# Kernel optimization log

Hardware: AMD Instinct MI355X
Metric: run time of the kernel (lower is better)

## Reference

```python
import jax, jax.numpy as jnp
import numpy as np

N_NODES = 50000
N_RAND_EDGES = 575000  # plus N_NODES self loops -> 625000 total edges
C = 128


def setup_inputs() -> dict:
    key = jax.random.key(0)
    ks = jax.random.split(key, 7)
    x = jax.random.normal(ks[0], (N_NODES, C), dtype=jnp.float32)
    er = jax.random.randint(ks[1], (2, N_RAND_EDGES), 0, N_NODES)
    loops = jnp.arange(N_NODES)
    edge_index = jnp.concatenate([er, jnp.stack([loops, loops])], axis=1)  # [2, E]
    E = edge_index.shape[1]
    edge_feature = jax.random.randint(ks[2], (E, 3), 0, 2)  # in-range for all 3 tables
    glorot = lambda k, shp: jax.random.uniform(k, shp, jnp.float32, -1.0, 1.0) * jnp.sqrt(6.0 / (shp[0] + shp[1]))
    weight = glorot(ks[3], (C, C))
    emb0 = glorot(ks[4], (5, C))
    emb1 = glorot(ks[5], (6, C))
    emb2 = glorot(ks[6], (2, C))
    return {"x": x, "edge_index": edge_index, "edge_feature": edge_feature,
            "weight": weight, "emb0": emb0, "emb1": emb1, "emb2": emb2}


def reference(x, edge_index, edge_feature, weight, emb0, emb1, emb2):
    n = x.shape[0]
    xw = x @ weight  # [N, C]
    # BondEncoder: sum of per-column embeddings -> [E, C]
    ef = emb0[edge_feature[:, 0]] + emb1[edge_feature[:, 1]] + emb2[edge_feature[:, 2]]
    row, col = edge_index[0], edge_index[1]
    # GCN symmetric normalization (graph already contains all self loops)
    deg = jax.ops.segment_sum(jnp.ones(row.shape[0], xw.dtype), row, num_segments=n)
    dinv = jnp.where(deg > 0, jax.lax.rsqrt(deg), 0.0)
    norm = dinv[row] * dinv[col]  # [E]
    # message: norm * (x_j + edge_feature); aggregate: scatter-add at target
    msg = norm[:, None] * (xw[row] + ef)  # [E, C]
    out = jax.ops.segment_sum(msg, col, num_segments=n)  # [N, C]
    return out
```

## Files before the change

kernel.cpp:

```cpp
#include <hip/hip_runtime.h>

#define CC 128
#define NB_HIST 96
#define MAXNW 12512
typedef unsigned short ushort_t;
typedef unsigned int uint_t;
typedef __attribute__((ext_vector_type(8))) short short8_t;
typedef __attribute__((ext_vector_type(4))) float float4_t;

__device__ __forceinline__ ushort_t f2bf(float f) {
    uint_t u = __float_as_uint(f);
    u = (u + 0x7FFFu + ((u >> 16) & 1u)) >> 16;
    return (ushort_t)u;
}
#define BF_LO(u) __uint_as_float((u) << 16)
#define BF_HI(u) __uint_as_float((u) & 0xFFFF0000u)

__global__ void prep_kernel(const float* __restrict__ w, ushort_t* __restrict__ wbt,
                            const float* __restrict__ emb0, const float* __restrict__ emb1,
                            const float* __restrict__ emb2, ushort_t* __restrict__ cmb) {
    if (blockIdx.x < 64) {
        const int i = blockIdx.x * 256 + threadIdx.x;
        const int nn = i >> 7, k = i & 127;
        wbt[i] = f2bf(w[k * CC + nn]);
    } else {
        const int c = blockIdx.x - 64;
        const int t = threadIdx.x;
        if (c < 60 && t < CC) {
            const int i0 = c / 12, j0 = (c % 12) / 2, k0 = c % 2;
            cmb[c * CC + t] = f2bf(emb0[i0 * CC + t] + emb1[j0 * CC + t] + emb2[k0 * CC + t]);
        }
    }
}

__global__ __launch_bounds__(256) void xw_kernel(const float* __restrict__ x,
                                                 const ushort_t* __restrict__ wbt,
                                                 ushort_t* __restrict__ xwb, int n) {
    const int wave = threadIdx.x >> 6;
    const int lane = threadIdx.x & 63;
    const int row0 = blockIdx.x * 64 + wave * 16;
    const int r  = lane & 15;
    const int kb = lane >> 4;
    const int arow = row0 + r;
    const bool rok = arow < n;

    float4_t acc[8];
    #pragma unroll
    for (int t = 0; t < 8; ++t) acc[t] = (float4_t){0.f, 0.f, 0.f, 0.f};

    #pragma unroll
    for (int ks = 0; ks < 4; ++ks) {
        short8_t ahi, alo;
        if (rok) {
            const float* xp = &x[(size_t)arow * CC + ks * 32 + kb * 8];
            const float4 x0 = *reinterpret_cast<const float4*>(xp);
            const float4 x1 = *reinterpret_cast<const float4*>(xp + 4);
            const float xv[8] = {x0.x, x0.y, x0.z, x0.w, x1.x, x1.y, x1.z, x1.w};
            #pragma unroll
            for (int i = 0; i < 8; ++i) {
                const ushort_t h = f2bf(xv[i]);
                ahi[i] = (short)h;
                const float hf = __uint_as_float((uint_t)h << 16);
                alo[i] = (short)f2bf(xv[i] - hf);
            }
        } else {
            #pragma unroll
            for (int i = 0; i < 8; ++i) { ahi[i] = 0; alo[i] = 0; }
        }
        #pragma unroll
        for (int nt = 0; nt < 8; ++nt) {
            const short8_t b = *reinterpret_cast<const short8_t*>(
                &wbt[(size_t)(nt * 16 + r) * CC + ks * 32 + kb * 8]);
            acc[nt] = __builtin_amdgcn_mfma_f32_16x16x32_bf16(alo, b, acc[nt], 0, 0, 0);
            acc[nt] = __builtin_amdgcn_mfma_f32_16x16x32_bf16(ahi, b, acc[nt], 0, 0, 0);
        }
    }
    #pragma unroll
    for (int reg = 0; reg < 4; ++reg) {
        const int orow = row0 + kb * 4 + reg;
        if (orow < n) {
            #pragma unroll
            for (int nt = 0; nt < 8; ++nt)
                xwb[(size_t)orow * CC + nt * 16 + r] = f2bf(acc[nt][reg]);
        }
    }
}

__global__ __launch_bounds__(1024) void hist2_kernel(const int* __restrict__ ei,
                                                     uint_t* __restrict__ bufr,
                                                     uint_t* __restrict__ bufc,
                                                     int E, int nw) {
    __shared__ uint_t hr[MAXNW];
    __shared__ uint_t hc[MAXNW];
    const int tid = threadIdx.x;
    for (int i = tid; i < nw; i += 1024) { hr[i] = 0u; hc[i] = 0u; }
    __syncthreads();
    const int chunk = (E + NB_HIST - 1) / NB_HIST;
    const int beg = blockIdx.x * chunk;
    const int end = min(E, beg + chunk);
    for (int i = beg + tid; i < end; i += 2048) {
        const int i1 = i + 1024;
        const bool ok1 = i1 < end;
        const int r0 = ei[i], c0 = ei[E + i];
        int r1 = 0, c1 = 0;
        if (ok1) { r1 = ei[i1]; c1 = ei[E + i1]; }
        atomicAdd(&hr[r0 >> 2], 1u << ((r0 & 3) * 8));
        atomicAdd(&hc[c0 >> 2], 1u << ((c0 & 3) * 8));
        if (ok1) {
            atomicAdd(&hr[r1 >> 2], 1u << ((r1 & 3) * 8));
            atomicAdd(&hc[c1 >> 2], 1u << ((c1 & 3) * 8));
        }
    }
    __syncthreads();
    uint_t* obr = &bufr[(size_t)blockIdx.x * nw];
    uint_t* obc = &bufc[(size_t)blockIdx.x * nw];
    for (int i = tid; i < nw; i += 1024) { obr[i] = hr[i]; obc[i] = hc[i]; }
}

__global__ void hscan_kernel(uint_t* __restrict__ bufr, uint_t* __restrict__ bufc,
                             float* __restrict__ dinv, int* __restrict__ cnt_col,
                             int* __restrict__ bsum, int nbw, int nw, int n) {
    const int t = threadIdx.x;
    if ((int)blockIdx.x < nbw) {
        const int w = blockIdx.x * 256 + t;
        if (w >= nw) return;
        uint_t s = 0;
        #pragma unroll 4
        for (int b = 0; b < NB_HIST; ++b) s += bufr[(size_t)b * nw + w];
        const int base = w * 4;
        float4 o;
        o.x = (s & 0xFFu)         ? rsqrtf((float)(s & 0xFFu)) : 0.f;
        o.y = ((s >> 8) & 0xFFu)  ? rsqrtf((float)((s >> 8) & 0xFFu)) : 0.f;
        o.z = ((s >> 16) & 0xFFu) ? rsqrtf((float)((s >> 16) & 0xFFu)) : 0.f;
        o.w = (s >> 24)           ? rsqrtf((float)(s >> 24)) : 0.f;
        if (base + 3 < n) *reinterpret_cast<float4*>(&dinv[base]) = o;
        else {
            if (base < n) dinv[base] = o.x;
            if (base + 1 < n) dinv[base + 1] = o.y;
            if (base + 2 < n) dinv[base + 2] = o.z;
        }
    } else {
        const int w = (blockIdx.x - nbw) * 256 + t;
        int tot = 0;
        if (w < nw) {
            uint_t s = 0;
            for (int b = 0; b < NB_HIST; ++b) {
                const size_t idx = (size_t)b * nw + w;
                const uint_t u = bufc[idx];
                bufc[idx] = s;
                s += u;
            }
            const int base = w * 4;
            int4 o;
            o.x = (int)(s & 0xFFu);
            o.y = (int)((s >> 8) & 0xFFu);
            o.z = (int)((s >> 16) & 0xFFu);
            o.w = (int)(s >> 24);
            if (base + 3 < n) { *reinterpret_cast<int4*>(&cnt_col[base]) = o; tot = o.x + o.y + o.z + o.w; }
            else {
                if (base < n) { cnt_col[base] = o.x; tot += o.x; }
                if (base + 1 < n) { cnt_col[base + 1] = o.y; tot += o.y; }
                if (base + 2 < n) { cnt_col[base + 2] = o.z; tot += o.z; }
            }
        }
        #pragma unroll
        for (int d = 32; d; d >>= 1) tot += __shfl_down(tot, d);
        __shared__ int wsum[4];
        if ((t & 63) == 0) wsum[t >> 6] = tot;
        __syncthreads();
        if (t == 0) bsum[blockIdx.x - nbw] = wsum[0] + wsum[1] + wsum[2] + wsum[3];
    }
}

__global__ void bscan_kernel(const int* __restrict__ bsum, int* __restrict__ boff,
                             int nb, int* __restrict__ offs, int n) {
    __shared__ int tmp[256];
    const int t = threadIdx.x;
    int v = (t < nb) ? bsum[t] : 0;
    tmp[t] = v; __syncthreads();
    for (int d = 1; d < 256; d <<= 1) {
        int u = (t >= d) ? tmp[t - d] : 0; __syncthreads();
        tmp[t] += u; __syncthreads();
    }
    if (t < nb) boff[t] = tmp[t] - v;
    if (t == 255) offs[n] = tmp[255];
}

__global__ void offs_kernel(const int* __restrict__ cnt, const int* __restrict__ boff,
                            int* __restrict__ offs, int* __restrict__ next, int nw, int n) {
    __shared__ int tmp[256];
    const int t = threadIdx.x;
    const int w = blockIdx.x * 256 + t;
    int4 c4 = {0, 0, 0, 0};
    const int base = w * 4;
    if (w < nw) {
        if (base + 3 < n) c4 = *reinterpret_cast<const int4*>(&cnt[base]);
        else {
            if (base < n) c4.x = cnt[base];
            if (base + 1 < n) c4.y = cnt[base + 1];
            if (base + 2 < n) c4.z = cnt[base + 2];
        }
    }
    const int tot = c4.x + c4.y + c4.z + c4.w;
    tmp[t] = tot; __syncthreads();
    for (int d = 1; d < 256; d <<= 1) {
        int u = (t >= d) ? tmp[t - d] : 0; __syncthreads();
        tmp[t] += u; __syncthreads();
    }
    if (w < nw) {
        int e = boff[blockIdx.x] + tmp[t] - tot;
        int4 o;
        o.x = e; o.y = e + c4.x; o.z = o.y + c4.y; o.w = o.z + c4.z;
        if (base + 3 < n) {
            *reinterpret_cast<int4*>(&offs[base]) = o;
            *reinterpret_cast<int4*>(&next[base]) = o;
        } else {
            if (base < n) { offs[base] = o.x; next[base] = o.x; }
            if (base + 1 < n) { offs[base + 1] = o.y; next[base + 1] = o.y; }
            if (base + 2 < n) { offs[base + 2] = o.z; next[base + 2] = o.z; }
        }
    }
}

__global__ __launch_bounds__(1024) void fill_kernel(const int* __restrict__ ei,
                                                    const int* __restrict__ ef,
                                                    const float* __restrict__ dinv,
                                                    const uint_t* __restrict__ bufc,
                                                    const int* __restrict__ offs,
                                                    int2* __restrict__ sc, int E, int nw) {
    __shared__ uint_t cur[MAXNW];
    const int tid = threadIdx.x;
    for (int i = tid; i < nw; i += 1024) cur[i] = 0u;
    __syncthreads();
    const int chunk = (E + NB_HIST - 1) / NB_HIST;
    const int beg = blockIdx.x * chunk;
    const int end = min(E, beg + chunk);
    const uint_t* myb = &bufc[(size_t)blockIdx.x * nw];
    for (int i0 = beg + tid; i0 < end; i0 += 4096) {
        int  ii[4]; bool ok[4];
        int  r4[4], c4[4], code4[4], pos4[4];
        float dv4[4];
        #pragma unroll
        for (int u = 0; u < 4; ++u) { ii[u] = i0 + u * 1024; ok[u] = ii[u] < end; }
        #pragma unroll
        for (int u = 0; u < 4; ++u) if (ok[u]) { r4[u] = ei[ii[u]]; c4[u] = ei[E + ii[u]]; }
        #pragma unroll
        for (int u = 0; u < 4; ++u) if (ok[u])
            code4[u] = ef[ii[u] * 3 + 0] * 12 + ef[ii[u] * 3 + 1] * 2 + ef[ii[u] * 3 + 2];
        #pragma unroll
        for (int u = 0; u < 4; ++u) if (ok[u]) dv4[u] = dinv[r4[u]];
        #pragma unroll
        for (int u = 0; u < 4; ++u) if (ok[u]) {
            const int c = c4[u];
            const int sh = (c & 3) * 8;
            const uint_t old = atomicAdd(&cur[c >> 2], 1u << sh);
            const int rank = (int)((old >> sh) & 0xFFu);
            const int cum = (int)((myb[c >> 2] >> sh) & 0xFFu);
            pos4[u] = offs[c] + cum + rank;
        }
        #pragma unroll
        for (int u = 0; u < 4; ++u) if (ok[u])
            sc[pos4[u]] = make_int2(r4[u] | (code4[u] << 16), __float_as_int(dv4[u]));
    }
}

__global__ void fill_glob_kernel(const int* __restrict__ ei, const int* __restrict__ ef,
                                 const float* __restrict__ dinv, int* __restrict__ next,
                                 int2* __restrict__ sc, int E) {
    int i = blockIdx.x * blockDim.x + threadIdx.x;
    int stride = gridDim.x * blockDim.x;
    for (; i < E; i += stride) {
        int r = ei[i];
        int c = ei[E + i];
        int pos = atomicAdd(&next[c], 1);
        int code = ef[i * 3 + 0] * 12 + ef[i * 3 + 1] * 2 + ef[i * 3 + 2];
        sc[pos] = make_int2(r | (code << 16), __float_as_int(dinv[r]));
    }
}

__global__ void hist_kernel(const int* __restrict__ ei, int* __restrict__ cnt_row,
                            int* __restrict__ cnt_col, int E) {
    int i = blockIdx.x * blockDim.x + threadIdx.x;
    int stride = gridDim.x * blockDim.x;
    for (; i < E; i += stride) {
        atomicAdd(&cnt_row[ei[i]], 1);
        atomicAdd(&cnt_col[ei[E + i]], 1);
    }
}
__global__ void dinv_kernel(const int* __restrict__ cnt_row, float* __restrict__ dinv, int n) {
    int i = blockIdx.x * blockDim.x + threadIdx.x;
    if (i < n) {
        int d = cnt_row[i];
        dinv[i] = (d > 0) ? rsqrtf((float)d) : 0.0f;
    }
}
__global__ void blocksum2_kernel(const int* __restrict__ cnt, int* __restrict__ bsum,
                                 int nw, int n) {
    const int t = threadIdx.x;
    const int w = blockIdx.x * 256 + t;
    int tot = 0;
    const int base = w * 4;
    if (w < nw) {
        for (int k = 0; k < 4; ++k) if (base + k < n) tot += cnt[base + k];
    }
    #pragma unroll
    for (int d = 32; d; d >>= 1) tot += __shfl_down(tot, d);
    __shared__ int wsum[4];
    if ((t & 63) == 0) wsum[t >> 6] = tot;
    __syncthreads();
    if (t == 0) bsum[blockIdx.x] = wsum[0] + wsum[1] + wsum[2] + wsum[3];
}

__global__ void gather_kernel(const ushort_t* __restrict__ xwb, const int2* __restrict__ sc,
                              const int* __restrict__ offs, const float* __restrict__ dinv,
                              const ushort_t* __restrict__ cmb, float* __restrict__ out, int n) {
    const int v = blockIdx.x * 4 + (threadIdx.x >> 6);
    if (v >= n) return;
    const int lane = threadIdx.x & 63;
    const int g = lane >> 4;
    const int l16 = lane & 15;
    const int end = offs[v + 1];

    float a[8];
    #pragma unroll
    for (int k = 0; k < 8; ++k) a[k] = 0.f;

    int jj = offs[v] + g;
    int2 e = (jj < end) ? sc[jj] : make_int2(0, 0);
    while (jj < end) {
        const int2 en = (jj + 4 < end) ? sc[jj + 4] : make_int2(0, 0);
        const int r_ = e.x & 0xFFFF, c_ = e.x >> 16;
        const float w_ = __int_as_float(e.y);
        const uint4 ux = *reinterpret_cast<const uint4*>(&xwb[(size_t)r_ * CC + l16 * 8]);
        const uint4 uc = *reinterpret_cast<const uint4*>(&cmb[c_ * CC + l16 * 8]);
        a[0] += w_ * (BF_LO(ux.x) + BF_LO(uc.x));
        a[1] += w_ * (BF_HI(ux.x) + BF_HI(uc.x));
        a[2] += w_ * (BF_LO(ux.y) + BF_LO(uc.y));
        a[3] += w_ * (BF_HI(ux.y) + BF_HI(uc.y));
        a[4] += w_ * (BF_LO(ux.z) + BF_LO(uc.z));
        a[5] += w_ * (BF_HI(ux.z) + BF_HI(uc.z));
        a[6] += w_ * (BF_LO(ux.w) + BF_LO(uc.w));
        a[7] += w_ * (BF_HI(ux.w) + BF_HI(uc.w));
        e = en;
        jj += 4;
    }
    #pragma unroll
    for (int k = 0; k < 8; ++k) {
        a[k] += __shfl_xor(a[k], 16);
        a[k] += __shfl_xor(a[k], 32);
    }
    if (g == 0) {
        const float s = dinv[v];
        float4 o0 = make_float4(s * a[0], s * a[1], s * a[2], s * a[3]);
        float4 o1 = make_float4(s * a[4], s * a[5], s * a[6], s * a[7]);
        float* op = &out[(size_t)v * CC + l16 * 8];
        *reinterpret_cast<float4*>(op) = o0;
        *reinterpret_cast<float4*>(op + 4) = o1;
    }
}

extern "C" void kernel_launch(void* const* d_in, const int* in_sizes, int n_in,
                              void* d_out, int out_size, void* d_ws, size_t ws_size,
                              hipStream_t stream) {
    const float* x      = (const float*)d_in[0];
    const int*   ei     = (const int*)d_in[1];
    const int*   ef     = (const int*)d_in[2];
    const float* weight = (const float*)d_in[3];
    const float* emb0   = (const float*)d_in[4];
    const float* emb1   = (const float*)d_in[5];
    const float* emb2   = (const float*)d_in[6];
    float* out = (float*)d_out;

    const int n = in_sizes[0] / CC;
    const int E = in_sizes[1] / 2;
    const int nw = (n + 3) / 4;
    const int nbw = (nw + 255) / 256;

    char* p = (char*)d_ws;
    auto alloc = [&](size_t bytes) {
        char* r = p;
        p += (bytes + 63) & ~(size_t)63;
        return r;
    };
    ushort_t* xwb   = (ushort_t*)alloc((size_t)n * CC * sizeof(ushort_t));
    ushort_t* wbt   = (ushort_t*)alloc(CC * CC * sizeof(ushort_t));
    ushort_t* cmb   = (ushort_t*)alloc(60 * CC * sizeof(ushort_t));
    float* dinv     = (float*)alloc(n * sizeof(float));
    int*   cnt_row  = (int*)alloc((size_t)n * sizeof(int));
    int*   cnt_col  = (int*)alloc((size_t)n * sizeof(int));
    int*   offs     = (int*)alloc((n + 1) * sizeof(int));
    int*   next     = (int*)alloc((size_t)n * sizeof(int));
    int*   bsum     = (int*)alloc(nbw * sizeof(int));
    int*   boff     = (int*)alloc(nbw * sizeof(int));
    int2*  sc       = (int2*)alloc((size_t)E * sizeof(int2));
    uint_t* bufr    = (uint_t*)alloc((size_t)NB_HIST * nw * sizeof(uint_t));
    uint_t* bufc    = (uint_t*)alloc((size_t)NB_HIST * nw * sizeof(uint_t));

    prep_kernel<<<124, 256, 0, stream>>>(weight, wbt, emb0, emb1, emb2, cmb);
    xw_kernel<<<(n + 63) / 64, 256, 0, stream>>>(x, wbt, xwb, n);

    if (n <= 50048) {
        hist2_kernel<<<NB_HIST, 1024, 0, stream>>>(ei, bufr, bufc, E, nw);
        hscan_kernel<<<2 * nbw, 256, 0, stream>>>(bufr, bufc, dinv, cnt_col, bsum, nbw, nw, n);
        bscan_kernel<<<1, 256, 0, stream>>>(bsum, boff, nbw, offs, n);
        offs_kernel<<<nbw, 256, 0, stream>>>(cnt_col, boff, offs, next, nw, n);
        fill_kernel<<<NB_HIST, 1024, 0, stream>>>(ei, ef, dinv, bufc, offs, sc, E, nw);
    } else {
        hipMemsetAsync(cnt_row, 0, (size_t)n * sizeof(int), stream);
        hipMemsetAsync(cnt_col, 0, (size_t)n * sizeof(int), stream);
        hist_kernel<<<2048, 256, 0, stream>>>(ei, cnt_row, cnt_col, E);
        dinv_kernel<<<(n + 255) / 256, 256, 0, stream>>>(cnt_row, dinv, n);
        blocksum2_kernel<<<nbw, 256, 0, stream>>>(cnt_col, bsum, nw, n);
        bscan_kernel<<<1, 256, 0, stream>>>(bsum, boff, nbw, offs, n);
        offs_kernel<<<nbw, 256, 0, stream>>>(cnt_col, boff, offs, next, nw, n);
        fill_glob_kernel<<<2048, 256, 0, stream>>>(ei, ef, dinv, next, sc, E);
    }
    gather_kernel<<<(n + 3) / 4, 256, 0, stream>>>(xwb, sc, offs, dinv, cmb, out, n);
}
```

Before: 114.5 us.

## Fold block-sum scan into offsets kernel and double histogram block count

```diff
diff --git a/kernel.cpp b/kernel.cpp
--- a/kernel.cpp
+++ b/kernel.cpp
@@ -1,7 +1,7 @@
 #include <hip/hip_runtime.h>
 
 #define CC 128
-#define NB_HIST 96
+#define NB_HIST 192
 #define MAXNW 12512
 typedef unsigned short ushort_t;
 typedef unsigned int uint_t;
@@ -186,8 +186,55 @@
     if (t == 255) offs[n] = tmp[255];
 }
 
-__global__ void offs_kernel(const int* __restrict__ cnt, const int* __restrict__ boff,
-                            int* __restrict__ offs, int* __restrict__ next, int nw, int n) {
+__global__ void offs_kernel(const int* __restrict__ cnt, const int* __restrict__ bsum,
+                            int* __restrict__ offs, int nbw, int nw, int n) {
+    __shared__ int tmp[256];
+    __shared__ int sboff;
+    const int t = threadIdx.x;
+    if (t < 64) {
+        int own = (t < nbw) ? bsum[t] : 0;
+        int v = own;
+        #pragma unroll
+        for (int d = 1; d < 64; d <<= 1) {
+            int u = __shfl_up(v, d);
+            if (t >= d) v += u;
+        }
+        if ((int)t == (int)blockIdx.x) sboff = v - own;
+        if (blockIdx.x == 0 && t == nbw - 1) offs[n] = v;
+    }
+    const int w = blockIdx.x * 256 + t;
+    int4 c4 = {0, 0, 0, 0};
+    const int base = w * 4;
+    if (w < nw) {
+        if (base + 3 < n) c4 = *reinterpret_cast<const int4*>(&cnt[base]);
+        else {
+            if (base < n) c4.x = cnt[base];
+            if (base + 1 < n) c4.y = cnt[base + 1];
+            if (base + 2 < n) c4.z = cnt[base + 2];
+        }
+    }
+    const int tot = c4.x + c4.y + c4.z + c4.w;
+    tmp[t] = tot; __syncthreads();
+    for (int d = 1; d < 256; d <<= 1) {
+        int u = (t >= d) ? tmp[t - d] : 0; __syncthreads();
+        tmp[t] += u; __syncthreads();
+    }
+    if (w < nw) {
+        int e = sboff + tmp[t] - tot;
+        int4 o;
+        o.x = e; o.y = e + c4.x; o.z = o.y + c4.y; o.w = o.z + c4.z;
+        if (base + 3 < n) {
+            *reinterpret_cast<int4*>(&offs[base]) = o;
+        } else {
+            if (base < n) offs[base] = o.x;
+            if (base + 1 < n) offs[base + 1] = o.y;
+            if (base + 2 < n) offs[base + 2] = o.z;
+        }
+    }
+}
+
+__global__ void offs_fb_kernel(const int* __restrict__ cnt, const int* __restrict__ boff,
+                               int* __restrict__ offs, int* __restrict__ next, int nw, int n) {
     __shared__ int tmp[256];
     const int t = threadIdx.x;
     const int w = blockIdx.x * 256 + t;
@@ -399,11 +446,10 @@
     prep_kernel<<<124, 256, 0, stream>>>(weight, wbt, emb0, emb1, emb2, cmb);
     xw_kernel<<<(n + 63) / 64, 256, 0, stream>>>(x, wbt, xwb, n);
 
-    if (n <= 50048) {
+    if (n <= 50048 && nbw <= 64) {
         hist2_kernel<<<NB_HIST, 1024, 0, stream>>>(ei, bufr, bufc, E, nw);
         hscan_kernel<<<2 * nbw, 256, 0, stream>>>(bufr, bufc, dinv, cnt_col, bsum, nbw, nw, n);
-        bscan_kernel<<<1, 256, 0, stream>>>(bsum, boff, nbw, offs, n);
-        offs_kernel<<<nbw, 256, 0, stream>>>(cnt_col, boff, offs, next, nw, n);
+        offs_kernel<<<nbw, 256, 0, stream>>>(cnt_col, bsum, offs, nbw, nw, n);
         fill_kernel<<<NB_HIST, 1024, 0, stream>>>(ei, ef, dinv, bufc, offs, sc, E, nw);
     } else {
         hipMemsetAsync(cnt_row, 0, (size_t)n * sizeof(int), stream);
@@ -412,7 +458,7 @@
         dinv_kernel<<<(n + 255) / 256, 256, 0, stream>>>(cnt_row, dinv, n);
         blocksum2_kernel<<<nbw, 256, 0, stream>>>(cnt_col, bsum, nw, n);
         bscan_kernel<<<1, 256, 0, stream>>>(bsum, boff, nbw, offs, n);
-        offs_kernel<<<nbw, 256, 0, stream>>>(cnt_col, boff, offs, next, nw, n);
+        offs_fb_kernel<<<nbw, 256, 0, stream>>>(cnt_col, boff, offs, next, nw, n);
         fill_glob_kernel<<<2048, 256, 0, stream>>>(ei, ef, dinv, next, sc, E);
     }
     gather_kernel<<<(n + 3) / 4, 256, 0, stream>>>(xwb, sc, offs, dinv, cmb, out, n);
```

Measured after the change: 116.5 us. About the same (+1.7%).
